# Optimization experiments

Measured on AMD Instinct MI355X. Metric: run time of the kernel, lower is better.

Reference implementation:

```python
import jax, jax.numpy as jnp
import numpy as np

BLOCK_SIZE = 4096
EMBED_SIZE = 1024
HEAD_SIZE = 128


def setup_inputs() -> dict:
    key = jax.random.key(0)
    kx, kq, kk, kv = jax.random.split(key, 4)
    B, T = 8, BLOCK_SIZE
    x = jax.random.normal(kx, (B, T, EMBED_SIZE), dtype=jnp.float32)
    # nn.Linear(embed, head, bias=False): weight (head, embed); y = x @ W.T
    scale = 1.0 / np.sqrt(EMBED_SIZE)
    Wq = jax.random.uniform(kq, (HEAD_SIZE, EMBED_SIZE), dtype=jnp.float32, minval=-scale, maxval=scale)
    Wk = jax.random.uniform(kk, (HEAD_SIZE, EMBED_SIZE), dtype=jnp.float32, minval=-scale, maxval=scale)
    Wv = jax.random.uniform(kv, (HEAD_SIZE, EMBED_SIZE), dtype=jnp.float32, minval=-scale, maxval=scale)
    return {"x": x, "Wq": Wq, "Wk": Wk, "Wv": Wv}


def reference(x, Wq, Wk, Wv):
    B, T, C = x.shape
    q = jnp.einsum('btc,hc->bth', x, Wq)  # (B,T,H)
    k = jnp.einsum('btc,hc->bth', x, Wk)
    v = jnp.einsum('btc,hc->bth', x, Wv)
    scale = jnp.asarray(Wq.shape[0], x.dtype) ** -0.5
    wei = jnp.einsum('bth,bsh->bts', q, k) * scale  # (B,T,T)
    causal = jnp.tril(jnp.ones((T, T), dtype=bool))
    wei = jnp.where(causal, wei, -jnp.inf)
    wei = jax.nn.softmax(wei, axis=-1)
    out = jnp.einsum('bts,bsh->bth', wei, v)  # (B,T,H)
    return out
```

## Files before the change

kernel.cpp:

```cpp
#include <hip/hip_runtime.h>
#include <stdint.h>

typedef unsigned short u16;
typedef __attribute__((ext_vector_type(8))) short short8;
typedef __attribute__((ext_vector_type(4))) float f32x4;

#define B_ 8
#define T_ 4096
#define C_ 1024
#define H_ 128

#if __has_builtin(__builtin_amdgcn_exp2f)
#define EXP2(x) __builtin_amdgcn_exp2f(x)
#else
#define EXP2(x) exp2f(x)
#endif

__device__ __forceinline__ u16 f2bf(float f) {
  union { float f; uint32_t u; } v; v.f = f;
  uint32_t r = v.u + 0x7fffu + ((v.u >> 16) & 1u);
  return (u16)(r >> 16);
}

__device__ __forceinline__ u16 f2bf_rn(float f) {
  union { float f; uint32_t u; } v; v.f = f;
  return (u16)((v.u + 0x8000u) >> 16);
}

__device__ __forceinline__ void gl_lds16(const u16* g, u16* l) {
  __builtin_amdgcn_global_load_lds(
      (const __attribute__((address_space(1))) void*)g,
      (__attribute__((address_space(3))) void*)l, 16, 0, 0);
}

__global__ __launch_bounds__(256) void wconv_kernel(
    const float* __restrict__ Wq, const float* __restrict__ Wk,
    const float* __restrict__ Wv, u16* __restrict__ Wb) {
  int g = (blockIdx.x * 256 + threadIdx.x) * 8;
  int head = g >> 17;
  int off  = g & 131071;
  const float* W = (head == 0) ? Wq : (head == 1) ? Wk : Wv;
  float s = (head == 0) ? 0.12751743342f : 1.0f;
  float4 a = *(const float4*)(W + off);
  float4 b = *(const float4*)(W + off + 4);
  u16 o[8] = {f2bf(a.x * s), f2bf(a.y * s), f2bf(a.z * s), f2bf(a.w * s),
              f2bf(b.x * s), f2bf(b.y * s), f2bf(b.z * s), f2bf(b.w * s)};
  *(uint4*)(Wb + g) = *(const uint4*)o;
}

__global__ __launch_bounds__(256, 2) void proj_kernel(
    const float* __restrict__ x, const u16* __restrict__ Wb,
    u16* __restrict__ qo, u16* __restrict__ ko, u16* __restrict__ vto) {
  __shared__ u16 Wl[384 * 64];
  __shared__ u16 Xl[64 * 72];

  const int bm   = blockIdx.x;
  const int tid  = threadIdx.x;
  const int wave = tid >> 6;
  const int lane = tid & 63;
  const int m    = lane & 15;
  const int q4   = lane >> 4;

  f32x4 acc[4][6] = {};

  const int xrow = tid >> 2, xc16 = (tid & 3) * 16;
  const u16* gW = Wb + (size_t)(wave * 96 + (lane >> 3)) * C_ +
                  (((lane & 7) ^ (lane >> 3)) << 3);
  const float* gX = x + (size_t)(bm * 64 + xrow) * C_ + xc16;

  for (int kc = 0; kc < C_; kc += 64) {
    __syncthreads();
    #pragma unroll
    for (int j = 0; j < 12; ++j)
      gl_lds16(gW + kc + (size_t)(j * 8) * C_, &Wl[(wave * 96 + j * 8) * 64]);
    {
      const float* xp = gX + kc;
      float4 a = *(const float4*)xp;
      float4 b = *(const float4*)(xp + 4);
      float4 c = *(const float4*)(xp + 8);
      float4 d = *(const float4*)(xp + 12);
      u16 o[16] = {f2bf_rn(a.x), f2bf_rn(a.y), f2bf_rn(a.z), f2bf_rn(a.w),
                   f2bf_rn(b.x), f2bf_rn(b.y), f2bf_rn(b.z), f2bf_rn(b.w),
                   f2bf_rn(c.x), f2bf_rn(c.y), f2bf_rn(c.z), f2bf_rn(c.w),
                   f2bf_rn(d.x), f2bf_rn(d.y), f2bf_rn(d.z), f2bf_rn(d.w)};
      *(uint4*)&Xl[xrow * 72 + xc16]     = *(const uint4*)&o[0];
      *(uint4*)&Xl[xrow * 72 + xc16 + 8] = *(const uint4*)&o[8];
    }
    __syncthreads();

    #pragma unroll
    for (int kb = 0; kb < 2; ++kb) {
      short8 af[4];
      #pragma unroll
      for (int s = 0; s < 4; ++s)
        af[s] = *(const short8*)&Xl[(s * 16 + m) * 72 + kb * 32 + q4 * 8];
      #pragma unroll
      for (int nb = 0; nb < 6; ++nb) {
        short8 bf = *(const short8*)&Wl[(wave * 96 + nb * 16 + m) * 64 +
                                        (((kb * 4 + q4) ^ (m & 7)) << 3)];
        #pragma unroll
        for (int s = 0; s < 4; ++s)
          acc[s][nb] =
              __builtin_amdgcn_mfma_f32_16x16x32_bf16(af[s], bf, acc[s][nb], 0, 0, 0);
      }
    }
  }

  #pragma unroll
  for (int s = 0; s < 4; ++s) {
    const int rowoff = s * 16 + q4 * 4;
    #pragma unroll
    for (int nb = 0; nb < 6; ++nb) {
      int col = wave * 96 + nb * 16 + m;
      f32x4 a = acc[s][nb];
      if (col < 128) {
        #pragma unroll
        for (int r = 0; r < 4; ++r)
          qo[(size_t)(bm * 64 + rowoff + r) * H_ + col] = f2bf(a[r]);
      } else if (col < 256) {
        #pragma unroll
        for (int r = 0; r < 4; ++r)
          ko[(size_t)(bm * 64 + rowoff + r) * H_ + (col - 128)] = f2bf(a[r]);
      } else {
        int b = bm >> 6;
        int t = (bm & 63) * 64 + rowoff;
        u16* vp = vto + (size_t)b * H_ * T_ + (size_t)(col - 256) * T_ + t;
        #pragma unroll
        for (int r = 0; r < 4; ++r) vp[r] = f2bf(a[r]);
      }
    }
  }
}

__global__ __launch_bounds__(256, 2) void attn_kernel(
    const u16* __restrict__ q, const u16* __restrict__ k,
    const u16* __restrict__ vt, float* __restrict__ out,
    float* __restrict__ po, float* __restrict__ pl) {
  __shared__ u16 Kl[2][64 * 128];
  __shared__ u16 Vl[2][128 * 64];
  __shared__ u16 Pl[4][2][16 * 64];

  const int bid   = blockIdx.x;
  const int batch = bid & 7;
  const int c     = bid >> 3;
  int Q, ck;
  if (c < 24)      { Q = 31 - c / 3;        ck = c % 3; }
  else if (c < 40) { Q = 23 - (c - 24) / 2; ck = (c - 24) & 1; }
  else if (c < 48) { Q = 15 - (c - 40);     ck = 0; }
  else { int t = c - 48; int qm = 7 - (t >> 2);
         Q = qm + (t & 3) * 8; ck = Q >> 3; }
  const int k0   = ck * 16;
  const int kend = min(k0 + 16, 2 * Q + 2);
  const bool single = (Q < 8);

  const int tid  = threadIdx.x;
  const int wave = tid >> 6;
  const int lane = tid & 63;
  const int m    = lane & 15;
  const int q4   = lane >> 4;

  const size_t bbase = (size_t)batch * T_ * H_;
  const u16* vbase   = vt + (size_t)batch * H_ * T_;

  short8 qf[2][4];
  #pragma unroll
  for (int si = 0; si < 2; ++si) {
    const u16* qp = q + bbase + (size_t)(Q * 128 + wave * 32 + si * 16 + m) * H_;
    #pragma unroll
    for (int kb = 0; kb < 4; ++kb)
      qf[si][kb] = *(const short8*)(qp + kb * 32 + q4 * 8);
  }

  const u16* gK[4];
  const u16* gV[4];
  #pragma unroll
  for (int j = 0; j < 4; ++j) {
    int r = wave * 16 + j * 4 + (lane >> 4);
    gK[j] = k + bbase + (size_t)r * H_ + (((lane & 15) ^ (r & 7)) << 3);
    int h = wave * 32 + j * 8 + (lane >> 3);
    gV[j] = vbase + (size_t)h * T_ + (((lane & 7) ^ (h & 7)) << 3);
  }

#define STAGE(bi, KT)                                                         \
  {                                                                           \
    u16* kd = &Kl[bi][wave * 16 * 128];                                       \
    const size_t ko_ = (size_t)(KT) * (64 * H_);                              \
    _Pragma("unroll") for (int j = 0; j < 4; ++j)                             \
        gl_lds16(gK[j] + ko_, kd + j * 4 * 128);                              \
    u16* vd = &Vl[bi][wave * 32 * 64];                                        \
    const size_t vo_ = (size_t)(KT) * 64;                                     \
    _Pragma("unroll") for (int j = 0; j < 4; ++j)                             \
        gl_lds16(gV[j] + vo_, vd + j * 8 * 64);                               \
  }

  float li[2][4] = {};
  f32x4 o[2][8] = {};
  const float NEGINF = -__builtin_inff();

  STAGE(0, k0);
  __syncthreads();
  int cur = 0;

  for (int kt = k0; kt < kend; ++kt) {
    if (kt + 1 < kend) STAGE(cur ^ 1, kt + 1);

    f32x4 sv[2][4];
    __builtin_amdgcn_s_setprio(1);
    #pragma unroll
    for (int nb = 0; nb < 4; ++nb) {
      f32x4 a0 = {}, a1 = {};
      #pragma unroll
      for (int kb = 0; kb < 4; ++kb) {
        short8 kf = *(const short8*)&Kl[cur][(nb * 16 + m) * 128 +
                                             (((kb * 4 + q4) ^ (m & 7)) << 3)];
        a0 = __builtin_amdgcn_mfma_f32_16x16x32_bf16(qf[0][kb], kf, a0, 0, 0, 0);
        a1 = __builtin_amdgcn_mfma_f32_16x16x32_bf16(qf[1][kb], kf, a1, 0, 0, 0);
      }
      sv[0][nb] = a0; sv[1][nb] = a1;
    }
    __builtin_amdgcn_s_setprio(0);

    if ((kt >> 1) == Q) {
      #pragma unroll
      for (int si = 0; si < 2; ++si)
        #pragma unroll
        for (int nb = 0; nb < 4; ++nb)
          #pragma unroll
          for (int r = 0; r < 4; ++r) {
            int key = ((kt & 1) << 6) + nb * 16 + m;
            int row = wave * 32 + si * 16 + q4 * 4 + r;
            if (key > row) sv[si][nb][r] = NEGINF;
          }
    }

    #pragma unroll
    for (int si = 0; si < 2; ++si)
      #pragma unroll
      for (int nb = 0; nb < 4; ++nb)
        #pragma unroll
        for (int r = 0; r < 4; ++r) {
          float p = EXP2(sv[si][nb][r]);
          li[si][r] += p;
          int rr = q4 * 4 + r;
          Pl[wave][si][rr * 64 + (((nb * 2 + (m >> 3)) ^ (rr & 7)) << 3) +
                       (m & 7)] = f2bf_rn(p);
        }

    __asm__ __volatile__("s_waitcnt lgkmcnt(0)" ::: "memory");
    __builtin_amdgcn_sched_barrier(0);

    __builtin_amdgcn_s_setprio(1);
    #pragma unroll
    for (int kb2 = 0; kb2 < 2; ++kb2) {
      short8 pf0 = *(const short8*)&Pl[wave][0][m * 64 +
                                   (((kb2 * 4 + q4) ^ (m & 7)) << 3)];
      short8 pf1 = *(const short8*)&Pl[wave][1][m * 64 +
                                   (((kb2 * 4 + q4) ^ (m & 7)) << 3)];
      #pragma unroll
      for (int nb = 0; nb < 8; ++nb) {
        short8 vf = *(const short8*)&Vl[cur][(nb * 16 + m) * 64 +
                                             (((kb2 * 4 + q4) ^ (m & 7)) << 3)];
        o[0][nb] = __builtin_amdgcn_mfma_f32_16x16x32_bf16(pf0, vf, o[0][nb], 0, 0, 0);
        o[1][nb] = __builtin_amdgcn_mfma_f32_16x16x32_bf16(pf1, vf, o[1][nb], 0, 0, 0);
      }
    }
    __builtin_amdgcn_s_setprio(0);

    if (kt + 1 < kend) {
      __syncthreads();
      cur ^= 1;
    }
  }

  #pragma unroll
  for (int si = 0; si < 2; ++si)
    #pragma unroll
    for (int r = 0; r < 4; ++r) {
      float t0 = li[si][r];
      t0 += __shfl_xor(t0, 1, 64);
      t0 += __shfl_xor(t0, 2, 64);
      t0 += __shfl_xor(t0, 4, 64);
      t0 += __shfl_xor(t0, 8, 64);
      li[si][r] = t0;
    }

  if (single) {
    #pragma unroll
    for (int si = 0; si < 2; ++si) {
      float* op = out + bbase + (size_t)(Q * 128 + wave * 32 + si * 16) * H_;
      #pragma unroll
      for (int nb = 0; nb < 8; ++nb)
        #pragma unroll
        for (int r = 0; r < 4; ++r)
          op[(q4 * 4 + r) * H_ + nb * 16 + m] = o[si][nb][r] / li[si][r];
    }
  } else {
    const size_t slot = (size_t)(batch * 32 + Q) * 4 + ck;
    #pragma unroll
    for (int si = 0; si < 2; ++si) {
      float* pp = po + slot * 16384 + (size_t)(wave * 32 + si * 16) * 128;
      #pragma unroll
      for (int nb = 0; nb < 8; ++nb)
        #pragma unroll
        for (int r = 0; r < 4; ++r)
          pp[(q4 * 4 + r) * 128 + nb * 16 + m] = o[si][nb][r];
      if (m == 0) {
        #pragma unroll
        for (int r = 0; r < 4; ++r)
          pl[slot * 128 + wave * 32 + si * 16 + q4 * 4 + r] = li[si][r];
      }
    }
  }
}

__global__ __launch_bounds__(256) void combine_kernel(
    const float* __restrict__ po, const float* __restrict__ pl,
    float* __restrict__ out) {
  int gid = blockIdx.x * 256 + threadIdx.x;
  int h4  = (gid & 31) * 4;
  int tt  = (gid >> 5) & 4095;
  int b   = gid >> 17;
  int Q   = tt >> 7, row = tt & 127;
  if (Q < 8) return;
  int nc = (Q >> 3) + 1;
  float4 s = {0.f, 0.f, 0.f, 0.f};
  float l = 0.f;
  for (int ck = 0; ck < nc; ++ck) {
    size_t slot = (size_t)(b * 32 + Q) * 4 + ck;
    float4 p = *(const float4*)(po + slot * 16384 + row * 128 + h4);
    s.x += p.x; s.y += p.y; s.z += p.z; s.w += p.w;
    l += pl[slot * 128 + row];
  }
  float inv = 1.0f / l;
  float4 r; r.x = s.x * inv; r.y = s.y * inv; r.z = s.z * inv; r.w = s.w * inv;
  *(float4*)(out + ((size_t)b * T_ + tt) * H_ + h4) = r;
}

extern "C" void kernel_launch(void* const* d_in, const int* in_sizes, int n_in,
                              void* d_out, int out_size, void* d_ws,
                              size_t ws_size, hipStream_t stream) {
  const float* x  = (const float*)d_in[0];
  const float* Wq = (const float*)d_in[1];
  const float* Wk = (const float*)d_in[2];
  const float* Wv = (const float*)d_in[3];

  const size_t n = (size_t)B_ * T_ * H_;
  u16* qb  = (u16*)d_ws;
  u16* kb  = qb + n;
  u16* vtb = kb + n;
  u16* Wbb = vtb + n;
  float* po = (float*)(Wbb + 393216);
  float* pl = po + (size_t)1024 * 16384;

  wconv_kernel<<<dim3(192), dim3(256), 0, stream>>>(Wq, Wk, Wv, Wbb);
  proj_kernel<<<dim3(512), dim3(256), 0, stream>>>(x, Wbb, qb, kb, vtb);
  attn_kernel<<<dim3(640), dim3(256), 0, stream>>>(qb, kb, vtb, (float*)d_out, po, pl);
  combine_kernel<<<dim3(4096), dim3(256), 0, stream>>>(po, pl, (float*)d_out);
}
```

Before: 277.9 us.

## Read V fragments directly from global memory, drop V LDS staging, raise occupancy

```diff
diff --git a/kernel.cpp b/kernel.cpp
--- a/kernel.cpp
+++ b/kernel.cpp
@@ -132,12 +132,11 @@
   }
 }
 
-__global__ __launch_bounds__(256, 2) void attn_kernel(
+__global__ __launch_bounds__(256, 3) void attn_kernel(
     const u16* __restrict__ q, const u16* __restrict__ k,
     const u16* __restrict__ vt, float* __restrict__ out,
     float* __restrict__ po, float* __restrict__ pl) {
   __shared__ u16 Kl[2][64 * 128];
-  __shared__ u16 Vl[2][128 * 64];
   __shared__ u16 Pl[4][2][16 * 64];
 
   const int bid   = blockIdx.x;
@@ -172,14 +171,12 @@
   }
 
   const u16* gK[4];
-  const u16* gV[4];
   #pragma unroll
   for (int j = 0; j < 4; ++j) {
     int r = wave * 16 + j * 4 + (lane >> 4);
     gK[j] = k + bbase + (size_t)r * H_ + (((lane & 15) ^ (r & 7)) << 3);
-    int h = wave * 32 + j * 8 + (lane >> 3);
-    gV[j] = vbase + (size_t)h * T_ + (((lane & 7) ^ (h & 7)) << 3);
-  }
+  }
+  const u16* vlane = vbase + (size_t)m * T_ + q4 * 8;
 
 #define STAGE(bi, KT)                                                         \
   {                                                                           \
@@ -187,10 +184,6 @@
     const size_t ko_ = (size_t)(KT) * (64 * H_);                              \
     _Pragma("unroll") for (int j = 0; j < 4; ++j)                             \
         gl_lds16(gK[j] + ko_, kd + j * 4 * 128);                              \
-    u16* vd = &Vl[bi][wave * 32 * 64];                                        \
-    const size_t vo_ = (size_t)(KT) * 64;                                     \
-    _Pragma("unroll") for (int j = 0; j < 4; ++j)                             \
-        gl_lds16(gV[j] + vo_, vd + j * 8 * 64);                               \
   }
 
   float li[2][4] = {};
@@ -204,11 +197,12 @@
   for (int kt = k0; kt < kend; ++kt) {
     if (kt + 1 < kend) STAGE(cur ^ 1, kt + 1);
 
-    f32x4 sv[2][4];
-    __builtin_amdgcn_s_setprio(1);
+    const bool diag = ((kt >> 1) == Q);
+
     #pragma unroll
     for (int nb = 0; nb < 4; ++nb) {
       f32x4 a0 = {}, a1 = {};
+      __builtin_amdgcn_s_setprio(1);
       #pragma unroll
       for (int kb = 0; kb < 4; ++kb) {
         short8 kf = *(const short8*)&Kl[cur][(nb * 16 + m) * 128 +
@@ -216,40 +210,34 @@
         a0 = __builtin_amdgcn_mfma_f32_16x16x32_bf16(qf[0][kb], kf, a0, 0, 0, 0);
         a1 = __builtin_amdgcn_mfma_f32_16x16x32_bf16(qf[1][kb], kf, a1, 0, 0, 0);
       }
-      sv[0][nb] = a0; sv[1][nb] = a1;
-    }
-    __builtin_amdgcn_s_setprio(0);
-
-    if ((kt >> 1) == Q) {
-      #pragma unroll
-      for (int si = 0; si < 2; ++si)
-        #pragma unroll
-        for (int nb = 0; nb < 4; ++nb)
-          #pragma unroll
-          for (int r = 0; r < 4; ++r) {
-            int key = ((kt & 1) << 6) + nb * 16 + m;
-            int row = wave * 32 + si * 16 + q4 * 4 + r;
-            if (key > row) sv[si][nb][r] = NEGINF;
-          }
-    }
-
-    #pragma unroll
-    for (int si = 0; si < 2; ++si)
-      #pragma unroll
-      for (int nb = 0; nb < 4; ++nb)
+      __builtin_amdgcn_s_setprio(0);
+      if (diag) {
+        int key = ((kt & 1) << 6) + nb * 16 + m;
         #pragma unroll
         for (int r = 0; r < 4; ++r) {
-          float p = EXP2(sv[si][nb][r]);
-          li[si][r] += p;
-          int rr = q4 * 4 + r;
-          Pl[wave][si][rr * 64 + (((nb * 2 + (m >> 3)) ^ (rr & 7)) << 3) +
-                       (m & 7)] = f2bf_rn(p);
+          int row0 = wave * 32 + q4 * 4 + r;
+          if (key > row0)      a0[r] = NEGINF;
+          if (key > row0 + 16) a1[r] = NEGINF;
         }
+      }
+      #pragma unroll
+      for (int r = 0; r < 4; ++r) {
+        int rr = q4 * 4 + r;
+        int cc = (((nb * 2 + (m >> 3)) ^ (rr & 7)) << 3) + (m & 7);
+        float p0 = EXP2(a0[r]);
+        li[0][r] += p0;
+        Pl[wave][0][rr * 64 + cc] = f2bf_rn(p0);
+        float p1 = EXP2(a1[r]);
+        li[1][r] += p1;
+        Pl[wave][1][rr * 64 + cc] = f2bf_rn(p1);
+      }
+    }
 
     __asm__ __volatile__("s_waitcnt lgkmcnt(0)" ::: "memory");
     __builtin_amdgcn_sched_barrier(0);
 
     __builtin_amdgcn_s_setprio(1);
+    const u16* vkt = vlane + kt * 64;
     #pragma unroll
     for (int kb2 = 0; kb2 < 2; ++kb2) {
       short8 pf0 = *(const short8*)&Pl[wave][0][m * 64 +
@@ -258,8 +246,7 @@
                                    (((kb2 * 4 + q4) ^ (m & 7)) << 3)];
       #pragma unroll
       for (int nb = 0; nb < 8; ++nb) {
-        short8 vf = *(const short8*)&Vl[cur][(nb * 16 + m) * 64 +
-                                             (((kb2 * 4 + q4) ^ (m & 7)) << 3)];
+        short8 vf = *(const short8*)(vkt + (size_t)(nb * 16) * T_ + kb2 * 32);
         o[0][nb] = __builtin_amdgcn_mfma_f32_16x16x32_bf16(pf0, vf, o[0][nb], 0, 0, 0);
         o[1][nb] = __builtin_amdgcn_mfma_f32_16x16x32_bf16(pf1, vf, o[1][nb], 0, 0, 0);
       }
```

Measured after the change: 348.7 us. 25.5% more time.
